# Optimization experiments

Hardware: AMD Instinct MI355X
Metric: run time of the kernel (lower is better)

The kernel has to match this reference:

```python
import jax, jax.numpy as jnp
import numpy as np
from itertools import combinations

N_QUBITS = 8
PAIRS = list(combinations(range(N_QUBITS), 2))  # 28 qubit pairs -> 28 features/node

# qubit 0 = first tensor factor (most significant bit of the basis index)
CNOT01 = jnp.array([[1,0,0,0],[0,1,0,0],[0,0,0,1],[0,0,1,0]], dtype=jnp.complex64)  # control q0, target q1
CNOT10 = jnp.array([[1,0,0,0],[0,0,0,1],[0,0,1,0],[0,1,0,0]], dtype=jnp.complex64)  # control q1, target q0
I2 = jnp.eye(2, dtype=jnp.complex64)
HZ = jnp.array([1.0, -1.0, 1.0, -1.0], dtype=jnp.complex64)  # diag(I kron Z)


def _rx(t):
    c = jnp.cos(t / 2).astype(jnp.complex64)
    s = jnp.sin(t / 2).astype(jnp.complex64)
    return jnp.stack([jnp.stack([c, -1j * s]), jnp.stack([-1j * s, c])])


def _ry(t):
    c = jnp.cos(t / 2).astype(jnp.complex64)
    s = jnp.sin(t / 2).astype(jnp.complex64)
    return jnp.stack([jnp.stack([c, -s]), jnp.stack([s, c])])


def _rz(t):
    e = jnp.exp(-0.5j * t.astype(jnp.complex64))
    z = jnp.zeros((), jnp.complex64)
    return jnp.stack([jnp.stack([e, z]), jnp.stack([z, jnp.conj(e)])])


def _pair_unitary(p):  # p: [6] params for one qubit pair
    A = _rz(p[5]) @ _ry(p[4]) @ _rx(p[3]) @ _rz(p[2]) @ _ry(p[1]) @ _rx(p[0])
    return CNOT01 @ (CNOT10 @ jnp.kron(A, I2))  # [4,4]


def _quantum_features(x, qweight):
    """Batched version of the per-node amplitude encoding + 28 two-qubit circuits."""
    N = x.shape[0]
    psi = (x / jnp.linalg.norm(x, axis=1, keepdims=True)).astype(jnp.complex64)  # [N,256]
    psi8 = psi.reshape((N,) + (2,) * N_QUBITS)
    Us = jax.vmap(_pair_unitary)(qweight.reshape(len(PAIRS), 6))  # [28,4,4]
    cols = []
    for p, (a, b) in enumerate(PAIRS):
        perm = (0, 1 + a, 1 + b) + tuple(1 + q for q in range(N_QUBITS) if q not in (a, b))
        v = jnp.transpose(psi8, perm).reshape(N, 4, 2 ** (N_QUBITS - 2))  # [N,4,64]
        rho = jnp.einsum('nim,njm->nij', v, jnp.conj(v))  # reduced 2-qubit DM [N,4,4]
        U = Us[p]
        # <I kron Z> after U rho U^dagger, mapped to [0,1]
        e = jnp.einsum('a,ab,nbc,ac->n', HZ, U, rho, jnp.conj(U))
        cols.append((jnp.real(e) + 1.0) * 0.5)
    return jnp.stack(cols, axis=1).astype(jnp.float32)  # [N,28]


def reference(x, edge_index, qweight, W1, b1, W2, b2):
    N = x.shape[0]
    x_deal = _quantum_features(x, qweight)  # [N,28]
    # gcn_norm with added self loops, edge_weight = 1
    loop = jnp.arange(N)
    src = jnp.concatenate([edge_index[0], loop])
    dst = jnp.concatenate([edge_index[1], loop])
    w = jnp.ones(src.shape[0], dtype=jnp.float32)
    deg = jax.ops.segment_sum(w, dst, num_segments=N)
    dinv = jax.lax.rsqrt(jnp.maximum(deg, 1e-12))
    norm = dinv[src] * w * dinv[dst]
    out = jax.ops.segment_sum(norm[:, None] * x_deal[src], dst, num_segments=N)  # [N,28]
    out = jax.nn.relu(out)
    g = (out.T @ out).reshape(1, 28 * 28)  # [1,784]
    h = jax.nn.relu(g @ W1.T + b1)
    return jax.nn.sigmoid(h @ W2.T + b2)  # [1,1]


def setup_inputs() -> dict:
    N, F, E = 50000, 256, 1600000
    key = jax.random.key(0)
    ks = jax.random.split(key, 6)
    x = jax.random.normal(ks[0], (N, F), dtype=jnp.float32)
    edge_index = jax.random.randint(ks[1], (2, E), 0, N, dtype=jnp.int64)
    qweight = jax.random.uniform(ks[2], (168,), dtype=jnp.float32) * (2.0 * np.pi)
    W1 = jax.random.normal(ks[3], (128, 784), dtype=jnp.float32) * 0.03
    b1 = jnp.zeros((128,), dtype=jnp.float32)
    W2 = jax.random.normal(ks[4], (1, 128), dtype=jnp.float32) * 0.08
    b2 = jnp.zeros((1,), dtype=jnp.float32)
    return {"x": x, "edge_index": edge_index, "qweight": qweight,
            "W1": W1, "b1": b1, "W2": W2, "b2": b2}
```

## Files before the change

kernel.cpp:

```cpp
#include <hip/hip_runtime.h>
#include <hip/hip_fp16.h>
#include <math.h>

#define N_NODES 50000
#define N_EDGES 1600000
#define BSHIFT 6
#define NB_BUCKETS 782
#define PART_CHUNK 8192
#define NCHUNK 196
#define CAP 3072
#define ZSTRIDE 32
#define GREP 16

template<int CTRL>
__device__ inline float dpp_mov(float x){
    return __int_as_float(__builtin_amdgcn_update_dpp(0, __float_as_int(x), CTRL, 0xf, 0xf, false));
}
__device__ inline float wave_sum_dpp(float x){
    x += dpp_mov<0x111>(x);
    x += dpp_mov<0x112>(x);
    x += dpp_mov<0x114>(x);
    x += dpp_mov<0x118>(x);
    x += dpp_mov<0x142>(x);
    x += dpp_mov<0x143>(x);
    return x;
}
__device__ inline float lane63(float x){
    return __int_as_float(__builtin_amdgcn_readlane(__float_as_int(x), 63));
}
#define DPP_XOR1 0xB1
#define DPP_XOR2 0x4E

struct C2 { float x, y; };
__device__ inline C2 mkc(float x, float y){ C2 r; r.x=x; r.y=y; return r; }
__device__ inline C2 cmul(C2 a, C2 b){ return mkc(a.x*b.x - a.y*b.y, a.x*b.y + a.y*b.x); }
__device__ inline C2 cadd(C2 a, C2 b){ return mkc(a.x+b.x, a.y+b.y); }

__global__ __launch_bounds__(256) void k_init(const float* __restrict__ qw,
        const void* __restrict__ ei, float4* __restrict__ cmat,
        int* __restrict__ flag, int* __restrict__ bucketFill, float* __restrict__ G){
    int t = threadIdx.x;
    for (int i = t; i < NB_BUCKETS; i += 256) bucketFill[i] = 0;
    for (int i = t; i < GREP*784; i += 256) G[i] = 0.f;
    if (t == 255){
        const long long* e64 = (const long long*)ei;
        int ok = 1;
        for (int i = 0; i < 64; i++){
            long long v = e64[i];
            if (v < 0 || v >= N_NODES) ok = 0;
        }
        flag[0] = ok;
    }
    if (t < 28){
        int p = t;
        int a = 0; { int rem = p, q = 0; while (rem >= 7 - q){ rem -= 7 - q; q++; } a = q; }
        C2 M00 = mkc(1,0), M01 = mkc(0,0), M10 = mkc(0,0), M11 = mkc(1,0);
        for (int k = 0; k < 6; k++){
            float th = 0.5f * qw[p*6 + k];
            float s, c; sincosf(th, &s, &c);
            C2 R00, R01, R10, R11;
            int type = k % 3;
            if (type == 0){
                R00 = mkc(c,0); R01 = mkc(0,-s); R10 = mkc(0,-s); R11 = mkc(c,0);
            } else if (type == 1){
                R00 = mkc(c,0); R01 = mkc(-s,0); R10 = mkc(s,0); R11 = mkc(c,0);
            } else {
                R00 = mkc(c,-s); R01 = mkc(0,0); R10 = mkc(0,0); R11 = mkc(c,s);
            }
            C2 N00 = cadd(cmul(R00,M00), cmul(R01,M10));
            C2 N01 = cadd(cmul(R00,M01), cmul(R01,M11));
            C2 N10 = cadd(cmul(R10,M00), cmul(R11,M10));
            C2 N11 = cadd(cmul(R10,M01), cmul(R11,M11));
            M00=N00; M01=N01; M10=N10; M11=N11;
        }
        float B00  = (M00.x*M00.x + M00.y*M00.y) - (M10.x*M10.x + M10.y*M10.y);
        float B11  = (M01.x*M01.x + M01.y*M01.y) - (M11.x*M11.x + M11.y*M11.y);
        float B01r = (M00.x*M01.x + M00.y*M01.y) - (M10.x*M11.x + M10.y*M11.y);
        cmat[p] = make_float4(0.5f + 0.5f*B11, 0.5f*(B00 - B11), B01r, (float)a);
    }
}

__device__ inline int get_edge(const void* ei, int is64, long long idx){
    if (is64) return (int)((const long long*)ei)[idx];
    return ((const int*)ei)[idx];
}

__global__ __launch_bounds__(1024) void k_part(const void* __restrict__ ei,
        const int* __restrict__ flag, int* __restrict__ bucketFill,
        unsigned* __restrict__ pairs){
    __shared__ int hist[NB_BUCKETS];
    __shared__ int cntb[NB_BUCKETS];
    __shared__ int cursor[NB_BUCKETS];
    __shared__ int copyBase[NB_BUCKETS];
    __shared__ unsigned sorted[PART_CHUNK];
    int tid = threadIdx.x, c = blockIdx.x;
    long long base = (long long)c * PART_CHUNK;
    int cnt = (int)((N_EDGES - base < PART_CHUNK) ? (N_EDGES - base) : PART_CHUNK);
    int is64 = flag[0];
    unsigned ds[8], sr[8];
    #pragma unroll
    for (int k = 0; k < 8; k++){
        int i = tid + 1024*k;
        if (i < cnt){
            ds[k] = (unsigned)get_edge(ei, is64, (long long)N_EDGES + base + i);
            sr[k] = (unsigned)get_edge(ei, is64, base + i);
        } else ds[k] = 0xffffffffu;
    }
    if (tid < NB_BUCKETS) hist[tid] = 0;
    __syncthreads();
    #pragma unroll
    for (int k = 0; k < 8; k++)
        if (ds[k] != 0xffffffffu) atomicAdd(&hist[ds[k] >> BSHIFT], 1);
    __syncthreads();
    if (tid < NB_BUCKETS) cntb[tid] = hist[tid];
    __syncthreads();
    for (int ofs = 1; ofs < NB_BUCKETS; ofs <<= 1){
        int v = 0; bool a = tid < NB_BUCKETS;
        if (a) v = hist[tid] + (tid >= ofs ? hist[tid - ofs] : 0);
        __syncthreads();
        if (a) hist[tid] = v;
        __syncthreads();
    }
    if (tid < NB_BUCKETS){
        int cb = cntb[tid];
        int ls = hist[tid] - cb;
        int gbase = tid*CAP + atomicAdd(&bucketFill[tid], cb);
        copyBase[tid] = gbase - ls;
        cursor[tid] = ls;
    }
    __syncthreads();
    #pragma unroll
    for (int k = 0; k < 8; k++){
        if (ds[k] != 0xffffffffu){
            int pos = atomicAdd(&cursor[ds[k] >> BSHIFT], 1);
            sorted[pos] = (ds[k] << 16) | sr[k];
        }
    }
    __syncthreads();
    for (int i = tid; i < cnt; i += 1024){
        unsigned v = sorted[i];
        int b = (int)(v >> 22);
        pairs[copyBase[b] + i] = v;
    }
}

__global__ __launch_bounds__(256) void k_deg(const unsigned* __restrict__ pairs,
        const int* __restrict__ bucketFill, float* __restrict__ dinv){
    __shared__ int hist[64];
    int b = blockIdx.x, t = threadIdx.x;
    int s0 = b*CAP;
    int cnt = bucketFill[b];
    if (cnt > CAP) cnt = CAP;
    if (t < 64) hist[t] = 0;
    __syncthreads();
    for (int i = t; i < cnt; i += 256)
        atomicAdd(&hist[(pairs[s0 + i] >> 16) & 63], 1);
    __syncthreads();
    if (t < 64){
        int n = b*64 + t;
        if (n < N_NODES) dinv[n] = rsqrtf((float)(hist[t] + 1));
    }
}

__global__ __launch_bounds__(256) void k_feat(const float* __restrict__ x,
        const float* __restrict__ dinv, const float4* __restrict__ cmat,
        __half* __restrict__ z){
    int wave = threadIdx.x >> 6;
    int lane = threadIdx.x & 63;
    int n = blockIdx.x*4 + wave;
    const float4 v = ((const float4*)(x + (size_t)n*256))[lane];
    float persq = v.x*v.x + v.y*v.y + v.z*v.z + v.w*v.w;

    float red[15];
    red[0] = persq;
    red[1] = v.x*v.x + v.y*v.y;
    red[2] = v.x*v.z + v.y*v.w;
    {
        float px = dpp_mov<DPP_XOR1>(v.x), py = dpp_mov<DPP_XOR1>(v.y);
        float pz = dpp_mov<DPP_XOR1>(v.z), pw = dpp_mov<DPP_XOR1>(v.w);
        red[3] = v.x*px + v.y*py + v.z*pz + v.w*pw;
        red[9] = (lane & 1) ? 0.f : persq;
    }
    {
        float px = dpp_mov<DPP_XOR2>(v.x), py = dpp_mov<DPP_XOR2>(v.y);
        float pz = dpp_mov<DPP_XOR2>(v.z), pw = dpp_mov<DPP_XOR2>(v.w);
        red[4] = v.x*px + v.y*py + v.z*pz + v.w*pw;
        red[10] = (lane & 2) ? 0.f : persq;
    }
    #pragma unroll
    for (int j = 2; j < 6; j++){
        float px = __shfl_xor(v.x, 1 << j), py = __shfl_xor(v.y, 1 << j);
        float pz = __shfl_xor(v.z, 1 << j), pw = __shfl_xor(v.w, 1 << j);
        red[3 + j] = v.x*px + v.y*py + v.z*pz + v.w*pw;
        red[9 + j] = ((lane >> j) & 1) ? 0.0f : persq;
    }
    float S[15];
    #pragma unroll
    for (int k = 0; k < 15; k++) S[k] = lane63(wave_sum_dpp(red[k]));

    if (lane < 28){
        float4 cm = cmat[lane];
        int ap = (int)cm.w;
        float S0a = (ap==6) ? S[1] :
                    (ap==0 ? S[14] : ap==1 ? S[13] : ap==2 ? S[12] :
                     ap==3 ? S[11] : ap==4 ? S[10] : S[9]);
        float Xa  = (ap==6) ? S[2] :
                    0.5f*(ap==0 ? S[8] : ap==1 ? S[7] : ap==2 ? S[6] :
                          ap==3 ? S[5] : ap==4 ? S[4] : S[3]);
        float feat = cm.x + (cm.y*S0a + cm.z*Xa) / S[0];
        z[(size_t)n*ZSTRIDE + lane] = __float2half(dinv[n] * feat);
    } else if (lane < 32){
        z[(size_t)n*ZSTRIDE + lane] = __float2half(0.f);
    }
}

__device__ inline void acc_pack(unsigned u, float& a, float& b){
    float2 f = __half22float2(__builtin_bit_cast(__half2, u));
    a += f.x; b += f.y;
}
__device__ inline void acc_row(const uint4* rp, float* acc ){
    uint4 w0 = rp[0], w1 = rp[1], w2 = rp[2], w3 = rp[3];
    acc_pack(w0.x, acc[0],  acc[1]);  acc_pack(w0.y, acc[2],  acc[3]);
    acc_pack(w0.z, acc[4],  acc[5]);  acc_pack(w0.w, acc[6],  acc[7]);
    acc_pack(w1.x, acc[8],  acc[9]);  acc_pack(w1.y, acc[10], acc[11]);
    acc_pack(w1.z, acc[12], acc[13]); acc_pack(w1.w, acc[14], acc[15]);
    acc_pack(w2.x, acc[16], acc[17]); acc_pack(w2.y, acc[18], acc[19]);
    acc_pack(w2.z, acc[20], acc[21]); acc_pack(w2.w, acc[22], acc[23]);
    acc_pack(w3.x, acc[24], acc[25]); acc_pack(w3.y, acc[26], acc[27]);
    acc_pack(w3.z, acc[28], acc[29]); acc_pack(w3.w, acc[30], acc[31]);
}

__global__ __launch_bounds__(512) void k_bucket(const unsigned* __restrict__ pairs,
        const int* __restrict__ bucketFill, const __half* __restrict__ z,
        const float* __restrict__ dinv, float* __restrict__ G){
    __shared__ unsigned short sorted[CAP];
    __shared__ int hist[64];
    __shared__ int cursor[64];
    __shared__ int begs[64];
    __shared__ int cnts[64];
    __shared__ float srow[64*28];
    int b = blockIdx.x, t = threadIdx.x;
    int s0 = b*CAP;
    int cnt = bucketFill[b];
    if (cnt > CAP) cnt = CAP;
    if (t < 64) hist[t] = 0;
    __syncthreads();
    for (int i = t; i < cnt; i += 512){
        unsigned v = pairs[s0 + i];
        atomicAdd(&hist[(v >> 16) & 63], 1);
    }
    __syncthreads();
    int mycnt = (t < 64) ? hist[t] : 0;
    for (int ofs = 1; ofs < 64; ofs <<= 1){
        int nv = 0;
        if (t < 64) nv = hist[t] + (t >= ofs ? hist[t - ofs] : 0);
        __syncthreads();
        if (t < 64) hist[t] = nv;
        __syncthreads();
    }
    if (t < 64){
        cursor[t] = hist[t] - mycnt;
        begs[t]   = hist[t] - mycnt;
        cnts[t]   = mycnt;
    }
    __syncthreads();
    for (int i = t; i < cnt; i += 512){
        unsigned v = pairs[s0 + i];
        int d = (v >> 16) & 63;
        int pos = atomicAdd(&cursor[d], 1);
        sorted[pos] = (unsigned short)(v & 0xffffu);
    }
    __syncthreads();

    int d = t >> 3, sub = t & 7;
    int n = b*64 + d;
    bool valid = n < N_NODES;
    float acc[32];
    #pragma unroll
    for (int k = 0; k < 32; k++) acc[k] = 0.f;
    if (valid){
        int beg = begs[d], end = beg + cnts[d];
        for (int i = beg + sub; i < end; i += 8){
            int src = sorted[i];
            acc_row((const uint4*)(z + (size_t)src*ZSTRIDE), acc);
        }
        if (sub == 7) acc_row((const uint4*)(z + (size_t)n*ZSTRIDE), acc);
    }
    #pragma unroll
    for (int k = 0; k < 32; k++){
        acc[k] += dpp_mov<DPP_XOR1>(acc[k]);
        acc[k] += dpp_mov<DPP_XOR2>(acc[k]);
        acc[k] += __shfl_xor(acc[k], 4);
    }
    if (sub == 0){
        float dv = valid ? dinv[n] : 0.f;
        #pragma unroll
        for (int k = 0; k < 28; k++)
            srow[d*28 + k] = fmaxf(acc[k]*dv, 0.f);
    }
    __syncthreads();

    if (t < 196){
        float* Gr = G + (size_t)(blockIdx.x & (GREP-1)) * 784;
        int ti = t / 14, tj = t % 14;
        int i0 = 2*ti, j0 = 2*tj;
        float c00 = 0.f, c01 = 0.f, c10 = 0.f, c11 = 0.f;
        for (int nn = 0; nn < 64; nn++){
            const float* r = srow + nn*28;
            float a0 = r[i0], a1 = r[i0+1], b0 = r[j0], b1 = r[j0+1];
            c00 += a0*b0; c01 += a0*b1; c10 += a1*b0; c11 += a1*b1;
        }
        atomicAdd(&Gr[(i0  )*28 + j0  ], c00);
        atomicAdd(&Gr[(i0  )*28 + j0+1], c01);
        atomicAdd(&Gr[(i0+1)*28 + j0  ], c10);
        atomicAdd(&Gr[(i0+1)*28 + j0+1], c11);
    }
}

__global__ __launch_bounds__(256) void k_mlp(const float* __restrict__ G,
        const float* __restrict__ W1, const float* __restrict__ b1,
        const float* __restrict__ W2, const float* __restrict__ b2,
        float* __restrict__ outp){
    __shared__ float Gs[784];
    __shared__ float part[256];
    __shared__ float h[128];
    int t = threadIdx.x;
    for (int i = t; i < 784; i += 256){
        float s = 0.f;
        #pragma unroll
        for (int r = 0; r < GREP; r++) s += G[r*784 + i];
        Gs[i] = s;
    }
    __syncthreads();
    int j = t & 127, halfsel = t >> 7;
    const float* w = W1 + (size_t)j*784 + halfsel*392;
    const float* g = Gs + halfsel*392;
    float s = 0.f;
    for (int i = 0; i < 392; i++) s += g[i] * w[i];
    part[t] = s;
    __syncthreads();
    if (t < 128) h[t] = fmaxf(part[t] + part[t+128] + b1[t], 0.f) * W2[t];
    __syncthreads();
    for (int ofs = 64; ofs > 0; ofs >>= 1){
        if (t < ofs) h[t] += h[t + ofs];
        __syncthreads();
    }
    if (t == 0) outp[0] = 1.f / (1.f + expf(-(h[0] + b2[0])));
}

extern "C" void kernel_launch(void* const* d_in, const int* in_sizes, int n_in,
                              void* d_out, int out_size, void* d_ws, size_t ws_size,
                              hipStream_t stream){
    const float* x  = (const float*)d_in[0];
    const void*  ei = d_in[1];
    const float* qw = (const float*)d_in[2];
    const float* W1 = (const float*)d_in[3];
    const float* b1 = (const float*)d_in[4];
    const float* W2 = (const float*)d_in[5];
    const float* b2 = (const float*)d_in[6];
    float* outp = (float*)d_out;

    char* base = (char*)d_ws;
    __half*         z     = (__half*)base;         base += (size_t)N_NODES*ZSTRIDE*2;
    unsigned*       pairs = (unsigned*)base;       base += (size_t)NB_BUCKETS*CAP*4;
    float*          dinv  = (float*)base;          base += (size_t)N_NODES*4;
    float4*         cmat  = (float4*)base;         base += 448;
    float*          G     = (float*)base;          base += GREP*784*4;
    int*            bucketFill = (int*)base;       base += 4096;
    int*            flag  = (int*)base;            base += 16;

    k_init<<<1, 256, 0, stream>>>(qw, ei, cmat, flag, bucketFill, G);
    k_part<<<NCHUNK, 1024, 0, stream>>>(ei, flag, bucketFill, pairs);
    k_deg<<<NB_BUCKETS, 256, 0, stream>>>(pairs, bucketFill, dinv);
    k_feat<<<N_NODES/4, 256, 0, stream>>>(x, dinv, cmat, z);
    k_bucket<<<NB_BUCKETS, 512, 0, stream>>>(pairs, bucketFill, z, dinv, G);
    k_mlp<<<1, 256, 0, stream>>>(G, W1, b1, W2, b2, outp);
}
```

Measured before the change: 176.4 us.

## Fuse edge partition with feature kernel and fold MLP into last bucket block

```diff
diff --git a/kernel.cpp b/kernel.cpp
--- a/kernel.cpp
+++ b/kernel.cpp
@@ -8,6 +8,7 @@
 #define NB_BUCKETS 782
 #define PART_CHUNK 8192
 #define NCHUNK 196
+#define FEAT_BLOCKS 3125
 #define CAP 3072
 #define ZSTRIDE 32
 #define GREP 16
@@ -38,10 +39,12 @@
 
 __global__ __launch_bounds__(256) void k_init(const float* __restrict__ qw,
         const void* __restrict__ ei, float4* __restrict__ cmat,
-        int* __restrict__ flag, int* __restrict__ bucketFill, float* __restrict__ G){
+        int* __restrict__ flag, int* __restrict__ bucketFill, float* __restrict__ G,
+        int* __restrict__ ticket){
     int t = threadIdx.x;
     for (int i = t; i < NB_BUCKETS; i += 256) bucketFill[i] = 0;
     for (int i = t; i < GREP*784; i += 256) G[i] = 0.f;
+    if (t == 0) ticket[0] = 0;
     if (t == 255){
         const long long* e64 = (const long long*)ei;
         int ok = 1;
@@ -85,62 +88,116 @@
     return ((const int*)ei)[idx];
 }
 
-__global__ __launch_bounds__(1024) void k_part(const void* __restrict__ ei,
+struct PartS {
+    int hist[NB_BUCKETS]; int cntb[NB_BUCKETS];
+    int cursor[NB_BUCKETS]; int copyBase[NB_BUCKETS];
+    unsigned sorted[PART_CHUNK];
+};
+
+__global__ __launch_bounds__(1024) void k_partfeat(
+        const float* __restrict__ x, const void* __restrict__ ei,
         const int* __restrict__ flag, int* __restrict__ bucketFill,
-        unsigned* __restrict__ pairs){
-    __shared__ int hist[NB_BUCKETS];
-    __shared__ int cntb[NB_BUCKETS];
-    __shared__ int cursor[NB_BUCKETS];
-    __shared__ int copyBase[NB_BUCKETS];
-    __shared__ unsigned sorted[PART_CHUNK];
-    int tid = threadIdx.x, c = blockIdx.x;
-    long long base = (long long)c * PART_CHUNK;
-    int cnt = (int)((N_EDGES - base < PART_CHUNK) ? (N_EDGES - base) : PART_CHUNK);
-    int is64 = flag[0];
-    unsigned ds[8], sr[8];
-    #pragma unroll
-    for (int k = 0; k < 8; k++){
-        int i = tid + 1024*k;
-        if (i < cnt){
-            ds[k] = (unsigned)get_edge(ei, is64, (long long)N_EDGES + base + i);
-            sr[k] = (unsigned)get_edge(ei, is64, base + i);
-        } else ds[k] = 0xffffffffu;
-    }
-    if (tid < NB_BUCKETS) hist[tid] = 0;
-    __syncthreads();
-    #pragma unroll
-    for (int k = 0; k < 8; k++)
-        if (ds[k] != 0xffffffffu) atomicAdd(&hist[ds[k] >> BSHIFT], 1);
-    __syncthreads();
-    if (tid < NB_BUCKETS) cntb[tid] = hist[tid];
-    __syncthreads();
-    for (int ofs = 1; ofs < NB_BUCKETS; ofs <<= 1){
-        int v = 0; bool a = tid < NB_BUCKETS;
-        if (a) v = hist[tid] + (tid >= ofs ? hist[tid - ofs] : 0);
-        __syncthreads();
-        if (a) hist[tid] = v;
-        __syncthreads();
-    }
-    if (tid < NB_BUCKETS){
-        int cb = cntb[tid];
-        int ls = hist[tid] - cb;
-        int gbase = tid*CAP + atomicAdd(&bucketFill[tid], cb);
-        copyBase[tid] = gbase - ls;
-        cursor[tid] = ls;
-    }
-    __syncthreads();
-    #pragma unroll
-    for (int k = 0; k < 8; k++){
-        if (ds[k] != 0xffffffffu){
-            int pos = atomicAdd(&cursor[ds[k] >> BSHIFT], 1);
-            sorted[pos] = (ds[k] << 16) | sr[k];
-        }
-    }
-    __syncthreads();
-    for (int i = tid; i < cnt; i += 1024){
-        unsigned v = sorted[i];
-        int b = (int)(v >> 22);
-        pairs[copyBase[b] + i] = v;
+        unsigned* __restrict__ pairs, const float4* __restrict__ cmat,
+        __half* __restrict__ z){
+    __shared__ PartS P;
+    int tid = threadIdx.x;
+    if (blockIdx.x < NCHUNK){
+        int c = blockIdx.x;
+        long long base = (long long)c * PART_CHUNK;
+        int cnt = (int)((N_EDGES - base < PART_CHUNK) ? (N_EDGES - base) : PART_CHUNK);
+        int is64 = flag[0];
+        unsigned ds[8], sr[8];
+        #pragma unroll
+        for (int k = 0; k < 8; k++){
+            int i = tid + 1024*k;
+            if (i < cnt){
+                ds[k] = (unsigned)get_edge(ei, is64, (long long)N_EDGES + base + i);
+                sr[k] = (unsigned)get_edge(ei, is64, base + i);
+            } else ds[k] = 0xffffffffu;
+        }
+        if (tid < NB_BUCKETS) P.hist[tid] = 0;
+        __syncthreads();
+        #pragma unroll
+        for (int k = 0; k < 8; k++)
+            if (ds[k] != 0xffffffffu) atomicAdd(&P.hist[ds[k] >> BSHIFT], 1);
+        __syncthreads();
+        if (tid < NB_BUCKETS) P.cntb[tid] = P.hist[tid];
+        __syncthreads();
+        for (int ofs = 1; ofs < NB_BUCKETS; ofs <<= 1){
+            int v = 0; bool a = tid < NB_BUCKETS;
+            if (a) v = P.hist[tid] + (tid >= ofs ? P.hist[tid - ofs] : 0);
+            __syncthreads();
+            if (a) P.hist[tid] = v;
+            __syncthreads();
+        }
+        if (tid < NB_BUCKETS){
+            int cb = P.cntb[tid];
+            int ls = P.hist[tid] - cb;
+            int gbase = tid*CAP + atomicAdd(&bucketFill[tid], cb);
+            P.copyBase[tid] = gbase - ls;
+            P.cursor[tid] = ls;
+        }
+        __syncthreads();
+        #pragma unroll
+        for (int k = 0; k < 8; k++){
+            if (ds[k] != 0xffffffffu){
+                int pos = atomicAdd(&P.cursor[ds[k] >> BSHIFT], 1);
+                P.sorted[pos] = (ds[k] << 16) | sr[k];
+            }
+        }
+        __syncthreads();
+        for (int i = tid; i < cnt; i += 1024){
+            unsigned v = P.sorted[i];
+            int b = (int)(v >> 22);
+            pairs[P.copyBase[b] + i] = v;
+        }
+    } else {
+        int wv = tid >> 6, lane = tid & 63;
+        int n = (blockIdx.x - NCHUNK)*16 + wv;
+        if (n < N_NODES){
+            const float4 v = ((const float4*)(x + (size_t)n*256))[lane];
+            float persq = v.x*v.x + v.y*v.y + v.z*v.z + v.w*v.w;
+            float red[15];
+            red[0] = persq;
+            red[1] = v.x*v.x + v.y*v.y;
+            red[2] = v.x*v.z + v.y*v.w;
+            {
+                float px = dpp_mov<DPP_XOR1>(v.x), py = dpp_mov<DPP_XOR1>(v.y);
+                float pz = dpp_mov<DPP_XOR1>(v.z), pw = dpp_mov<DPP_XOR1>(v.w);
+                red[3] = v.x*px + v.y*py + v.z*pz + v.w*pw;
+                red[9] = (lane & 1) ? 0.f : persq;
+            }
+            {
+                float px = dpp_mov<DPP_XOR2>(v.x), py = dpp_mov<DPP_XOR2>(v.y);
+                float pz = dpp_mov<DPP_XOR2>(v.z), pw = dpp_mov<DPP_XOR2>(v.w);
+                red[4] = v.x*px + v.y*py + v.z*pz + v.w*pw;
+                red[10] = (lane & 2) ? 0.f : persq;
+            }
+            #pragma unroll
+            for (int j = 2; j < 6; j++){
+                float px = __shfl_xor(v.x, 1 << j), py = __shfl_xor(v.y, 1 << j);
+                float pz = __shfl_xor(v.z, 1 << j), pw = __shfl_xor(v.w, 1 << j);
+                red[3 + j] = v.x*px + v.y*py + v.z*pz + v.w*pw;
+                red[9 + j] = ((lane >> j) & 1) ? 0.0f : persq;
+            }
+            float S[15];
+            #pragma unroll
+            for (int k = 0; k < 15; k++) S[k] = lane63(wave_sum_dpp(red[k]));
+            if (lane < 28){
+                float4 cm = cmat[lane];
+                int ap = (int)cm.w;
+                float S0a = (ap==6) ? S[1] :
+                            (ap==0 ? S[14] : ap==1 ? S[13] : ap==2 ? S[12] :
+                             ap==3 ? S[11] : ap==4 ? S[10] : S[9]);
+                float Xa  = (ap==6) ? S[2] :
+                            0.5f*(ap==0 ? S[8] : ap==1 ? S[7] : ap==2 ? S[6] :
+                                  ap==3 ? S[5] : ap==4 ? S[4] : S[3]);
+                float feat = cm.x + (cm.y*S0a + cm.z*Xa) / S[0];
+                z[(size_t)n*ZSTRIDE + lane] = __float2half(feat);
+            } else if (lane < 32){
+                z[(size_t)n*ZSTRIDE + lane] = __float2half(0.f);
+            }
+        }
     }
 }
 
@@ -162,113 +219,69 @@
     }
 }
 
-__global__ __launch_bounds__(256) void k_feat(const float* __restrict__ x,
-        const float* __restrict__ dinv, const float4* __restrict__ cmat,
-        __half* __restrict__ z){
-    int wave = threadIdx.x >> 6;
-    int lane = threadIdx.x & 63;
-    int n = blockIdx.x*4 + wave;
-    const float4 v = ((const float4*)(x + (size_t)n*256))[lane];
-    float persq = v.x*v.x + v.y*v.y + v.z*v.z + v.w*v.w;
-
-    float red[15];
-    red[0] = persq;
-    red[1] = v.x*v.x + v.y*v.y;
-    red[2] = v.x*v.z + v.y*v.w;
-    {
-        float px = dpp_mov<DPP_XOR1>(v.x), py = dpp_mov<DPP_XOR1>(v.y);
-        float pz = dpp_mov<DPP_XOR1>(v.z), pw = dpp_mov<DPP_XOR1>(v.w);
-        red[3] = v.x*px + v.y*py + v.z*pz + v.w*pw;
-        red[9] = (lane & 1) ? 0.f : persq;
-    }
-    {
-        float px = dpp_mov<DPP_XOR2>(v.x), py = dpp_mov<DPP_XOR2>(v.y);
-        float pz = dpp_mov<DPP_XOR2>(v.z), pw = dpp_mov<DPP_XOR2>(v.w);
-        red[4] = v.x*px + v.y*py + v.z*pz + v.w*pw;
-        red[10] = (lane & 2) ? 0.f : persq;
-    }
-    #pragma unroll
-    for (int j = 2; j < 6; j++){
-        float px = __shfl_xor(v.x, 1 << j), py = __shfl_xor(v.y, 1 << j);
-        float pz = __shfl_xor(v.z, 1 << j), pw = __shfl_xor(v.w, 1 << j);
-        red[3 + j] = v.x*px + v.y*py + v.z*pz + v.w*pw;
-        red[9 + j] = ((lane >> j) & 1) ? 0.0f : persq;
-    }
-    float S[15];
-    #pragma unroll
-    for (int k = 0; k < 15; k++) S[k] = lane63(wave_sum_dpp(red[k]));
-
-    if (lane < 28){
-        float4 cm = cmat[lane];
-        int ap = (int)cm.w;
-        float S0a = (ap==6) ? S[1] :
-                    (ap==0 ? S[14] : ap==1 ? S[13] : ap==2 ? S[12] :
-                     ap==3 ? S[11] : ap==4 ? S[10] : S[9]);
-        float Xa  = (ap==6) ? S[2] :
-                    0.5f*(ap==0 ? S[8] : ap==1 ? S[7] : ap==2 ? S[6] :
-                          ap==3 ? S[5] : ap==4 ? S[4] : S[3]);
-        float feat = cm.x + (cm.y*S0a + cm.z*Xa) / S[0];
-        z[(size_t)n*ZSTRIDE + lane] = __float2half(dinv[n] * feat);
-    } else if (lane < 32){
-        z[(size_t)n*ZSTRIDE + lane] = __float2half(0.f);
-    }
-}
-
-__device__ inline void acc_pack(unsigned u, float& a, float& b){
+__device__ inline void acc_pack(unsigned u, float w, float& a, float& b){
     float2 f = __half22float2(__builtin_bit_cast(__half2, u));
-    a += f.x; b += f.y;
-}
-__device__ inline void acc_row(const uint4* rp, float* acc ){
+    a = fmaf(w, f.x, a); b = fmaf(w, f.y, b);
+}
+__device__ inline void acc_row(float w, const uint4* rp, float* acc ){
     uint4 w0 = rp[0], w1 = rp[1], w2 = rp[2], w3 = rp[3];
-    acc_pack(w0.x, acc[0],  acc[1]);  acc_pack(w0.y, acc[2],  acc[3]);
-    acc_pack(w0.z, acc[4],  acc[5]);  acc_pack(w0.w, acc[6],  acc[7]);
-    acc_pack(w1.x, acc[8],  acc[9]);  acc_pack(w1.y, acc[10], acc[11]);
-    acc_pack(w1.z, acc[12], acc[13]); acc_pack(w1.w, acc[14], acc[15]);
-    acc_pack(w2.x, acc[16], acc[17]); acc_pack(w2.y, acc[18], acc[19]);
-    acc_pack(w2.z, acc[20], acc[21]); acc_pack(w2.w, acc[22], acc[23]);
-    acc_pack(w3.x, acc[24], acc[25]); acc_pack(w3.y, acc[26], acc[27]);
-    acc_pack(w3.z, acc[28], acc[29]); acc_pack(w3.w, acc[30], acc[31]);
-}
+    acc_pack(w0.x, w, acc[0],  acc[1]);  acc_pack(w0.y, w, acc[2],  acc[3]);
+    acc_pack(w0.z, w, acc[4],  acc[5]);  acc_pack(w0.w, w, acc[6],  acc[7]);
+    acc_pack(w1.x, w, acc[8],  acc[9]);  acc_pack(w1.y, w, acc[10], acc[11]);
+    acc_pack(w1.z, w, acc[12], acc[13]); acc_pack(w1.w, w, acc[14], acc[15]);
+    acc_pack(w2.x, w, acc[16], acc[17]); acc_pack(w2.y, w, acc[18], acc[19]);
+    acc_pack(w2.z, w, acc[20], acc[21]); acc_pack(w2.w, w, acc[22], acc[23]);
+    acc_pack(w3.x, w, acc[24], acc[25]); acc_pack(w3.y, w, acc[26], acc[27]);
+    acc_pack(w3.z, w, acc[28], acc[29]); acc_pack(w3.w, w, acc[30], acc[31]);
+}
+
+struct BucketS {
+    unsigned short sorted[CAP];
+    int hist[64]; int cursor[64]; int begs[64]; int cnts[64];
+    float srow[64*28];
+};
+struct MlpS { float Gs[784]; float prt[512]; float h[128]; };
+union BSMem { BucketS b; MlpS m; };
 
 __global__ __launch_bounds__(512) void k_bucket(const unsigned* __restrict__ pairs,
         const int* __restrict__ bucketFill, const __half* __restrict__ z,
-        const float* __restrict__ dinv, float* __restrict__ G){
-    __shared__ unsigned short sorted[CAP];
-    __shared__ int hist[64];
-    __shared__ int cursor[64];
-    __shared__ int begs[64];
-    __shared__ int cnts[64];
-    __shared__ float srow[64*28];
+        const float* __restrict__ dinv, float* __restrict__ G,
+        int* __restrict__ ticket,
+        const float* __restrict__ W1, const float* __restrict__ b1,
+        const float* __restrict__ W2, const float* __restrict__ b2,
+        float* __restrict__ outp){
+    __shared__ BSMem U;
+    __shared__ int lastS;
     int b = blockIdx.x, t = threadIdx.x;
     int s0 = b*CAP;
     int cnt = bucketFill[b];
     if (cnt > CAP) cnt = CAP;
-    if (t < 64) hist[t] = 0;
+    if (t < 64) U.b.hist[t] = 0;
     __syncthreads();
     for (int i = t; i < cnt; i += 512){
         unsigned v = pairs[s0 + i];
-        atomicAdd(&hist[(v >> 16) & 63], 1);
-    }
-    __syncthreads();
-    int mycnt = (t < 64) ? hist[t] : 0;
+        atomicAdd(&U.b.hist[(v >> 16) & 63], 1);
+    }
+    __syncthreads();
+    int mycnt = (t < 64) ? U.b.hist[t] : 0;
     for (int ofs = 1; ofs < 64; ofs <<= 1){
         int nv = 0;
-        if (t < 64) nv = hist[t] + (t >= ofs ? hist[t - ofs] : 0);
-        __syncthreads();
-        if (t < 64) hist[t] = nv;
+        if (t < 64) nv = U.b.hist[t] + (t >= ofs ? U.b.hist[t - ofs] : 0);
+        __syncthreads();
+        if (t < 64) U.b.hist[t] = nv;
         __syncthreads();
     }
     if (t < 64){
-        cursor[t] = hist[t] - mycnt;
-        begs[t]   = hist[t] - mycnt;
-        cnts[t]   = mycnt;
+        U.b.cursor[t] = U.b.hist[t] - mycnt;
+        U.b.begs[t]   = U.b.hist[t] - mycnt;
+        U.b.cnts[t]   = mycnt;
     }
     __syncthreads();
     for (int i = t; i < cnt; i += 512){
         unsigned v = pairs[s0 + i];
         int d = (v >> 16) & 63;
-        int pos = atomicAdd(&cursor[d], 1);
-        sorted[pos] = (unsigned short)(v & 0xffffu);
+        int pos = atomicAdd(&U.b.cursor[d], 1);
+        U.b.sorted[pos] = (unsigned short)(v & 0xffffu);
     }
     __syncthreads();
 
@@ -279,12 +292,13 @@
     #pragma unroll
     for (int k = 0; k < 32; k++) acc[k] = 0.f;
     if (valid){
-        int beg = begs[d], end = beg + cnts[d];
+        int beg = U.b.begs[d], end = beg + U.b.cnts[d];
         for (int i = beg + sub; i < end; i += 8){
-            int src = sorted[i];
-            acc_row((const uint4*)(z + (size_t)src*ZSTRIDE), acc);
-        }
-        if (sub == 7) acc_row((const uint4*)(z + (size_t)n*ZSTRIDE), acc);
+            int src = U.b.sorted[i];
+            acc_row(dinv[src], (const uint4*)(z + (size_t)src*ZSTRIDE), acc);
+        }
+        if (sub == 7)
+            acc_row(dinv[n], (const uint4*)(z + (size_t)n*ZSTRIDE), acc);
     }
     #pragma unroll
     for (int k = 0; k < 32; k++){
@@ -296,17 +310,17 @@
         float dv = valid ? dinv[n] : 0.f;
         #pragma unroll
         for (int k = 0; k < 28; k++)
-            srow[d*28 + k] = fmaxf(acc[k]*dv, 0.f);
+            U.b.srow[d*28 + k] = fmaxf(acc[k]*dv, 0.f);
     }
     __syncthreads();
 
     if (t < 196){
-        float* Gr = G + (size_t)(blockIdx.x & (GREP-1)) * 784;
+        float* Gr = G + (size_t)(b & (GREP-1)) * 784;
         int ti = t / 14, tj = t % 14;
         int i0 = 2*ti, j0 = 2*tj;
         float c00 = 0.f, c01 = 0.f, c10 = 0.f, c11 = 0.f;
         for (int nn = 0; nn < 64; nn++){
-            const float* r = srow + nn*28;
+            const float* r = U.b.srow + nn*28;
             float a0 = r[i0], a1 = r[i0+1], b0 = r[j0], b1 = r[j0+1];
             c00 += a0*b0; c01 += a0*b1; c10 += a1*b0; c11 += a1*b1;
         }
@@ -315,37 +329,38 @@
         atomicAdd(&Gr[(i0+1)*28 + j0  ], c10);
         atomicAdd(&Gr[(i0+1)*28 + j0+1], c11);
     }
-}
-
-__global__ __launch_bounds__(256) void k_mlp(const float* __restrict__ G,
-        const float* __restrict__ W1, const float* __restrict__ b1,
-        const float* __restrict__ W2, const float* __restrict__ b2,
-        float* __restrict__ outp){
-    __shared__ float Gs[784];
-    __shared__ float part[256];
-    __shared__ float h[128];
-    int t = threadIdx.x;
-    for (int i = t; i < 784; i += 256){
+
+    __threadfence();
+    __syncthreads();
+    if (t == 0) lastS = atomicAdd(ticket, 1);
+    __syncthreads();
+    if (lastS != NB_BUCKETS - 1) return;
+
+    for (int i = t; i < 784; i += 512){
         float s = 0.f;
         #pragma unroll
-        for (int r = 0; r < GREP; r++) s += G[r*784 + i];
-        Gs[i] = s;
-    }
-    __syncthreads();
-    int j = t & 127, halfsel = t >> 7;
-    const float* w = W1 + (size_t)j*784 + halfsel*392;
-    const float* g = Gs + halfsel*392;
+        for (int r = 0; r < GREP; r++)
+            s += __hip_atomic_load(&G[r*784 + i], __ATOMIC_RELAXED, __HIP_MEMORY_SCOPE_AGENT);
+        U.m.Gs[i] = s;
+    }
+    __syncthreads();
+    int j = t & 127, q = t >> 7;
+    const float* w = W1 + (size_t)j*784 + q*196;
+    const float* g = U.m.Gs + q*196;
     float s = 0.f;
-    for (int i = 0; i < 392; i++) s += g[i] * w[i];
-    part[t] = s;
-    __syncthreads();
-    if (t < 128) h[t] = fmaxf(part[t] + part[t+128] + b1[t], 0.f) * W2[t];
+    for (int i = 0; i < 196; i++) s += g[i] * w[i];
+    U.m.prt[t] = s;
+    __syncthreads();
+    if (t < 128){
+        float hv = U.m.prt[t] + U.m.prt[t+128] + U.m.prt[t+256] + U.m.prt[t+384] + b1[t];
+        U.m.h[t] = fmaxf(hv, 0.f) * W2[t];
+    }
     __syncthreads();
     for (int ofs = 64; ofs > 0; ofs >>= 1){
-        if (t < ofs) h[t] += h[t + ofs];
-        __syncthreads();
-    }
-    if (t == 0) outp[0] = 1.f / (1.f + expf(-(h[0] + b2[0])));
+        if (t < ofs) U.m.h[t] += U.m.h[t + ofs];
+        __syncthreads();
+    }
+    if (t == 0) outp[0] = 1.f / (1.f + expf(-(U.m.h[0] + b2[0])));
 }
 
 extern "C" void kernel_launch(void* const* d_in, const int* in_sizes, int n_in,
@@ -361,18 +376,18 @@
     float* outp = (float*)d_out;
 
     char* base = (char*)d_ws;
-    __half*         z     = (__half*)base;         base += (size_t)N_NODES*ZSTRIDE*2;
-    unsigned*       pairs = (unsigned*)base;       base += (size_t)NB_BUCKETS*CAP*4;
-    float*          dinv  = (float*)base;          base += (size_t)N_NODES*4;
-    float4*         cmat  = (float4*)base;         base += 448;
-    float*          G     = (float*)base;          base += GREP*784*4;
-    int*            bucketFill = (int*)base;       base += 4096;
-    int*            flag  = (int*)base;            base += 16;
-
-    k_init<<<1, 256, 0, stream>>>(qw, ei, cmat, flag, bucketFill, G);
-    k_part<<<NCHUNK, 1024, 0, stream>>>(ei, flag, bucketFill, pairs);
+    __half*   z     = (__half*)base;   base += (size_t)N_NODES*ZSTRIDE*2;
+    unsigned* pairs = (unsigned*)base; base += (size_t)NB_BUCKETS*CAP*4;
+    float*    dinv  = (float*)base;    base += (size_t)N_NODES*4;
+    float4*   cmat  = (float4*)base;   base += 448;
+    float*    G     = (float*)base;    base += GREP*784*4;
+    int*      bucketFill = (int*)base; base += 4096;
+    int*      flag  = (int*)base;      base += 16;
+    int*      ticket = (int*)base;     base += 16;
+
+    k_init<<<1, 256, 0, stream>>>(qw, ei, cmat, flag, bucketFill, G, ticket);
+    k_partfeat<<<NCHUNK + FEAT_BLOCKS, 1024, 0, stream>>>(x, ei, flag, bucketFill, pairs, cmat, z);
     k_deg<<<NB_BUCKETS, 256, 0, stream>>>(pairs, bucketFill, dinv);
-    k_feat<<<N_NODES/4, 256, 0, stream>>>(x, dinv, cmat, z);
-    k_bucket<<<NB_BUCKETS, 512, 0, stream>>>(pairs, bucketFill, z, dinv, G);
-    k_mlp<<<1, 256, 0, stream>>>(G, W1, b1, W2, b2, outp);
-}
+    k_bucket<<<NB_BUCKETS, 512, 0, stream>>>(pairs, bucketFill, z, dinv, G, ticket,
+                                             W1, b1, W2, b2, outp);
+}
```

Result: slower. 263.1 us (+49.2%).

## Merge edge partition and feature kernels into one launch, defer degree scaling

Applied to the files above, without the earlier changes.

```diff
diff --git a/kernel.cpp b/kernel.cpp
--- a/kernel.cpp
+++ b/kernel.cpp
@@ -8,6 +8,7 @@
 #define NB_BUCKETS 782
 #define PART_CHUNK 8192
 #define NCHUNK 196
+#define FEAT_BLOCKS 3125
 #define CAP 3072
 #define ZSTRIDE 32
 #define GREP 16
@@ -85,68 +86,124 @@
     return ((const int*)ei)[idx];
 }
 
-__global__ __launch_bounds__(1024) void k_part(const void* __restrict__ ei,
+struct PartS {
+    int hist[NB_BUCKETS]; int cntb[NB_BUCKETS];
+    int cursor[NB_BUCKETS]; int copyBase[NB_BUCKETS];
+    unsigned sorted[PART_CHUNK];
+};
+
+__global__ __launch_bounds__(1024) void k_partfeat(
+        const float* __restrict__ x, const void* __restrict__ ei,
         const int* __restrict__ flag, int* __restrict__ bucketFill,
-        unsigned* __restrict__ pairs){
-    __shared__ int hist[NB_BUCKETS];
-    __shared__ int cntb[NB_BUCKETS];
-    __shared__ int cursor[NB_BUCKETS];
-    __shared__ int copyBase[NB_BUCKETS];
-    __shared__ unsigned sorted[PART_CHUNK];
-    int tid = threadIdx.x, c = blockIdx.x;
-    long long base = (long long)c * PART_CHUNK;
-    int cnt = (int)((N_EDGES - base < PART_CHUNK) ? (N_EDGES - base) : PART_CHUNK);
-    int is64 = flag[0];
-    unsigned ds[8], sr[8];
-    #pragma unroll
-    for (int k = 0; k < 8; k++){
-        int i = tid + 1024*k;
-        if (i < cnt){
-            ds[k] = (unsigned)get_edge(ei, is64, (long long)N_EDGES + base + i);
-            sr[k] = (unsigned)get_edge(ei, is64, base + i);
-        } else ds[k] = 0xffffffffu;
-    }
-    if (tid < NB_BUCKETS) hist[tid] = 0;
-    __syncthreads();
-    #pragma unroll
-    for (int k = 0; k < 8; k++)
-        if (ds[k] != 0xffffffffu) atomicAdd(&hist[ds[k] >> BSHIFT], 1);
-    __syncthreads();
-    if (tid < NB_BUCKETS) cntb[tid] = hist[tid];
-    __syncthreads();
-    for (int ofs = 1; ofs < NB_BUCKETS; ofs <<= 1){
-        int v = 0; bool a = tid < NB_BUCKETS;
-        if (a) v = hist[tid] + (tid >= ofs ? hist[tid - ofs] : 0);
-        __syncthreads();
-        if (a) hist[tid] = v;
-        __syncthreads();
-    }
-    if (tid < NB_BUCKETS){
-        int cb = cntb[tid];
-        int ls = hist[tid] - cb;
-        int gbase = tid*CAP + atomicAdd(&bucketFill[tid], cb);
-        copyBase[tid] = gbase - ls;
-        cursor[tid] = ls;
-    }
-    __syncthreads();
-    #pragma unroll
-    for (int k = 0; k < 8; k++){
-        if (ds[k] != 0xffffffffu){
-            int pos = atomicAdd(&cursor[ds[k] >> BSHIFT], 1);
-            sorted[pos] = (ds[k] << 16) | sr[k];
-        }
-    }
-    __syncthreads();
-    for (int i = tid; i < cnt; i += 1024){
-        unsigned v = sorted[i];
-        int b = (int)(v >> 22);
-        pairs[copyBase[b] + i] = v;
-    }
-}
-
-__global__ __launch_bounds__(256) void k_deg(const unsigned* __restrict__ pairs,
-        const int* __restrict__ bucketFill, float* __restrict__ dinv){
+        unsigned* __restrict__ pairs, const float4* __restrict__ cmat,
+        __half* __restrict__ z){
+    __shared__ PartS P;
+    int tid = threadIdx.x;
+    if (blockIdx.x < NCHUNK){
+        int c = blockIdx.x;
+        long long base = (long long)c * PART_CHUNK;
+        int cnt = (int)((N_EDGES - base < PART_CHUNK) ? (N_EDGES - base) : PART_CHUNK);
+        int is64 = flag[0];
+        unsigned ds[8], sr[8];
+        #pragma unroll
+        for (int k = 0; k < 8; k++){
+            int i = tid + 1024*k;
+            if (i < cnt){
+                ds[k] = (unsigned)get_edge(ei, is64, (long long)N_EDGES + base + i);
+                sr[k] = (unsigned)get_edge(ei, is64, base + i);
+            } else ds[k] = 0xffffffffu;
+        }
+        if (tid < NB_BUCKETS) P.hist[tid] = 0;
+        __syncthreads();
+        #pragma unroll
+        for (int k = 0; k < 8; k++)
+            if (ds[k] != 0xffffffffu) atomicAdd(&P.hist[ds[k] >> BSHIFT], 1);
+        __syncthreads();
+        if (tid < NB_BUCKETS) P.cntb[tid] = P.hist[tid];
+        __syncthreads();
+        for (int ofs = 1; ofs < NB_BUCKETS; ofs <<= 1){
+            int v = 0; bool a = tid < NB_BUCKETS;
+            if (a) v = P.hist[tid] + (tid >= ofs ? P.hist[tid - ofs] : 0);
+            __syncthreads();
+            if (a) P.hist[tid] = v;
+            __syncthreads();
+        }
+        if (tid < NB_BUCKETS){
+            int cb = P.cntb[tid];
+            int ls = P.hist[tid] - cb;
+            int gbase = tid*CAP + atomicAdd(&bucketFill[tid], cb);
+            P.copyBase[tid] = gbase - ls;
+            P.cursor[tid] = ls;
+        }
+        __syncthreads();
+        #pragma unroll
+        for (int k = 0; k < 8; k++){
+            if (ds[k] != 0xffffffffu){
+                int pos = atomicAdd(&P.cursor[ds[k] >> BSHIFT], 1);
+                P.sorted[pos] = (ds[k] << 16) | sr[k];
+            }
+        }
+        __syncthreads();
+        for (int i = tid; i < cnt; i += 1024){
+            unsigned v = P.sorted[i];
+            int b = (int)(v >> 22);
+            pairs[P.copyBase[b] + i] = v;
+        }
+    } else {
+        int wv = tid >> 6, lane = tid & 63;
+        int n = (blockIdx.x - NCHUNK)*16 + wv;
+        if (n < N_NODES){
+            const float4 v = ((const float4*)(x + (size_t)n*256))[lane];
+            float persq = v.x*v.x + v.y*v.y + v.z*v.z + v.w*v.w;
+            float red[15];
+            red[0] = persq;
+            red[1] = v.x*v.x + v.y*v.y;
+            red[2] = v.x*v.z + v.y*v.w;
+            {
+                float px = dpp_mov<DPP_XOR1>(v.x), py = dpp_mov<DPP_XOR1>(v.y);
+                float pz = dpp_mov<DPP_XOR1>(v.z), pw = dpp_mov<DPP_XOR1>(v.w);
+                red[3] = v.x*px + v.y*py + v.z*pz + v.w*pw;
+                red[9] = (lane & 1) ? 0.f : persq;
+            }
+            {
+                float px = dpp_mov<DPP_XOR2>(v.x), py = dpp_mov<DPP_XOR2>(v.y);
+                float pz = dpp_mov<DPP_XOR2>(v.z), pw = dpp_mov<DPP_XOR2>(v.w);
+                red[4] = v.x*px + v.y*py + v.z*pz + v.w*pw;
+                red[10] = (lane & 2) ? 0.f : persq;
+            }
+            #pragma unroll
+            for (int j = 2; j < 6; j++){
+                float px = __shfl_xor(v.x, 1 << j), py = __shfl_xor(v.y, 1 << j);
+                float pz = __shfl_xor(v.z, 1 << j), pw = __shfl_xor(v.w, 1 << j);
+                red[3 + j] = v.x*px + v.y*py + v.z*pz + v.w*pw;
+                red[9 + j] = ((lane >> j) & 1) ? 0.0f : persq;
+            }
+            float S[15];
+            #pragma unroll
+            for (int k = 0; k < 15; k++) S[k] = lane63(wave_sum_dpp(red[k]));
+            if (lane < 28){
+                float4 cm = cmat[lane];
+                int ap = (int)cm.w;
+                float S0a = (ap==6) ? S[1] :
+                            (ap==0 ? S[14] : ap==1 ? S[13] : ap==2 ? S[12] :
+                             ap==3 ? S[11] : ap==4 ? S[10] : S[9]);
+                float Xa  = (ap==6) ? S[2] :
+                            0.5f*(ap==0 ? S[8] : ap==1 ? S[7] : ap==2 ? S[6] :
+                                  ap==3 ? S[5] : ap==4 ? S[4] : S[3]);
+                float feat = cm.x + (cm.y*S0a + cm.z*Xa) / S[0];
+                z[(size_t)n*ZSTRIDE + lane] = __float2half(feat);
+            } else if (lane < 32){
+                z[(size_t)n*ZSTRIDE + lane] = __float2half(0.f);
+            }
+        }
+    }
+}
+
+__global__ __launch_bounds__(256) void k_degscale(const unsigned* __restrict__ pairs,
+        const int* __restrict__ bucketFill, float* __restrict__ dinv,
+        __half* __restrict__ z){
     __shared__ int hist[64];
+    __shared__ float sdv[64];
     int b = blockIdx.x, t = threadIdx.x;
     int s0 = b*CAP;
     int cnt = bucketFill[b];
@@ -158,59 +215,19 @@
     __syncthreads();
     if (t < 64){
         int n = b*64 + t;
-        if (n < N_NODES) dinv[n] = rsqrtf((float)(hist[t] + 1));
-    }
-}
-
-__global__ __launch_bounds__(256) void k_feat(const float* __restrict__ x,
-        const float* __restrict__ dinv, const float4* __restrict__ cmat,
-        __half* __restrict__ z){
-    int wave = threadIdx.x >> 6;
-    int lane = threadIdx.x & 63;
-    int n = blockIdx.x*4 + wave;
-    const float4 v = ((const float4*)(x + (size_t)n*256))[lane];
-    float persq = v.x*v.x + v.y*v.y + v.z*v.z + v.w*v.w;
-
-    float red[15];
-    red[0] = persq;
-    red[1] = v.x*v.x + v.y*v.y;
-    red[2] = v.x*v.z + v.y*v.w;
-    {
-        float px = dpp_mov<DPP_XOR1>(v.x), py = dpp_mov<DPP_XOR1>(v.y);
-        float pz = dpp_mov<DPP_XOR1>(v.z), pw = dpp_mov<DPP_XOR1>(v.w);
-        red[3] = v.x*px + v.y*py + v.z*pz + v.w*pw;
-        red[9] = (lane & 1) ? 0.f : persq;
-    }
-    {
-        float px = dpp_mov<DPP_XOR2>(v.x), py = dpp_mov<DPP_XOR2>(v.y);
-        float pz = dpp_mov<DPP_XOR2>(v.z), pw = dpp_mov<DPP_XOR2>(v.w);
-        red[4] = v.x*px + v.y*py + v.z*pz + v.w*pw;
-        red[10] = (lane & 2) ? 0.f : persq;
-    }
-    #pragma unroll
-    for (int j = 2; j < 6; j++){
-        float px = __shfl_xor(v.x, 1 << j), py = __shfl_xor(v.y, 1 << j);
-        float pz = __shfl_xor(v.z, 1 << j), pw = __shfl_xor(v.w, 1 << j);
-        red[3 + j] = v.x*px + v.y*py + v.z*pz + v.w*pw;
-        red[9 + j] = ((lane >> j) & 1) ? 0.0f : persq;
-    }
-    float S[15];
-    #pragma unroll
-    for (int k = 0; k < 15; k++) S[k] = lane63(wave_sum_dpp(red[k]));
-
-    if (lane < 28){
-        float4 cm = cmat[lane];
-        int ap = (int)cm.w;
-        float S0a = (ap==6) ? S[1] :
-                    (ap==0 ? S[14] : ap==1 ? S[13] : ap==2 ? S[12] :
-                     ap==3 ? S[11] : ap==4 ? S[10] : S[9]);
-        float Xa  = (ap==6) ? S[2] :
-                    0.5f*(ap==0 ? S[8] : ap==1 ? S[7] : ap==2 ? S[6] :
-                          ap==3 ? S[5] : ap==4 ? S[4] : S[3]);
-        float feat = cm.x + (cm.y*S0a + cm.z*Xa) / S[0];
-        z[(size_t)n*ZSTRIDE + lane] = __float2half(dinv[n] * feat);
-    } else if (lane < 32){
-        z[(size_t)n*ZSTRIDE + lane] = __float2half(0.f);
+        float dv = rsqrtf((float)(hist[t] + 1));
+        sdv[t] = dv;
+        if (n < N_NODES) dinv[n] = dv;
+    }
+    __syncthreads();
+    __half2* zp = (__half2*)z + (size_t)b*64*(ZSTRIDE/2);
+    for (int i = t; i < 64*(ZSTRIDE/2); i += 256){
+        int d = i >> 4;
+        if (b*64 + d < N_NODES){
+            float2 f = __half22float2(zp[i]);
+            float dv = sdv[d];
+            zp[i] = __floats2half2_rn(f.x*dv, f.y*dv);
+        }
     }
 }
 
@@ -301,7 +318,7 @@
     __syncthreads();
 
     if (t < 196){
-        float* Gr = G + (size_t)(blockIdx.x & (GREP-1)) * 784;
+        float* Gr = G + (size_t)(b & (GREP-1)) * 784;
         int ti = t / 14, tj = t % 14;
         int i0 = 2*ti, j0 = 2*tj;
         float c00 = 0.f, c01 = 0.f, c10 = 0.f, c11 = 0.f;
@@ -361,18 +378,17 @@
     float* outp = (float*)d_out;
 
     char* base = (char*)d_ws;
-    __half*         z     = (__half*)base;         base += (size_t)N_NODES*ZSTRIDE*2;
-    unsigned*       pairs = (unsigned*)base;       base += (size_t)NB_BUCKETS*CAP*4;
-    float*          dinv  = (float*)base;          base += (size_t)N_NODES*4;
-    float4*         cmat  = (float4*)base;         base += 448;
-    float*          G     = (float*)base;          base += GREP*784*4;
-    int*            bucketFill = (int*)base;       base += 4096;
-    int*            flag  = (int*)base;            base += 16;
+    __half*   z     = (__half*)base;   base += (size_t)N_NODES*ZSTRIDE*2;
+    unsigned* pairs = (unsigned*)base; base += (size_t)NB_BUCKETS*CAP*4;
+    float*    dinv  = (float*)base;    base += (size_t)N_NODES*4;
+    float4*   cmat  = (float4*)base;   base += 448;
+    float*    G     = (float*)base;    base += GREP*784*4;
+    int*      bucketFill = (int*)base; base += 4096;
+    int*      flag  = (int*)base;      base += 16;
 
     k_init<<<1, 256, 0, stream>>>(qw, ei, cmat, flag, bucketFill, G);
-    k_part<<<NCHUNK, 1024, 0, stream>>>(ei, flag, bucketFill, pairs);
-    k_deg<<<NB_BUCKETS, 256, 0, stream>>>(pairs, bucketFill, dinv);
-    k_feat<<<N_NODES/4, 256, 0, stream>>>(x, dinv, cmat, z);
+    k_partfeat<<<NCHUNK + FEAT_BLOCKS, 1024, 0, stream>>>(x, ei, flag, bucketFill, pairs, cmat, z);
+    k_degscale<<<NB_BUCKETS, 256, 0, stream>>>(pairs, bucketFill, dinv, z);
     k_bucket<<<NB_BUCKETS, 512, 0, stream>>>(pairs, bucketFill, z, dinv, G);
     k_mlp<<<1, 256, 0, stream>>>(G, W1, b1, W2, b2, outp);
 }
```

After: 175.3 us, median of 2. No clear change (-0.6%).
